# Kernel tuning notes

Measured on AMD Instinct MI355X. Metric: run time of the kernel, lower is better.

The kernel has to match this reference:

```python
import jax, jax.numpy as jnp
import numpy as np

B, T, S, D, H = 2, 2048, 2048, 2048, 16
HD = D // H  # 128
SCALE = 1.0 / np.sqrt(HD)


def _rope(x, cos, sin):
    # x: [B,H,S,HD]; cos/sin: [1,1,S,HD//2]
    b, h, s, d = x.shape
    xs = x.reshape(b, h, s, d // 2, 2)
    x0, x1 = xs[..., 0], xs[..., 1]
    rot = jnp.stack([x0 * cos - x1 * sin, x1 * cos + x0 * sin], axis=-1)
    return rot.reshape(b, h, s, d)


def _split_heads(x):
    b, s, _ = x.shape
    return x.reshape(b, s, H, HD).transpose(0, 2, 1, 3)


def setup_inputs() -> dict:
    key = jax.random.key(0)
    ks = jax.random.split(key, 6)
    w_std = (1.0 / np.sqrt(2.0)) * np.sqrt(6.0 / (D + D))  # xavier_uniform with gain 1/sqrt(2)
    def xavier(k):
        return jax.random.uniform(k, (D, D), jnp.float32, -w_std, w_std)
    # rotary tables (standard inv-freq form)
    inv_freq = 1.0 / (10000.0 ** (np.arange(0, HD, 2, dtype=np.float32) / HD))  # [HD//2]
    ang = np.arange(T, dtype=np.float32)[:, None] * inv_freq[None, :]           # [T,HD//2]
    cos = jnp.asarray(np.cos(ang), jnp.float32)[None, None]  # [1,1,T,HD//2]
    sin = jnp.asarray(np.sin(ang), jnp.float32)[None, None]
    return {
        "hidden_states": jax.random.normal(ks[0], (B, T, D), jnp.float32),
        "encoder_hidden_states": jax.random.normal(ks[1], (B, S, D), jnp.float32),
        "Wq": xavier(ks[2]),
        "Wk": xavier(ks[3]),
        "Wv": xavier(ks[4]),
        "Wo": xavier(ks[5]),
        "cos_q": cos, "sin_q": sin,
        "cos_k": cos, "sin_k": sin,
    }


def reference(hidden_states, encoder_hidden_states, Wq, Wk, Wv, Wo,
              cos_q, sin_q, cos_k, sin_k):
    # Linear (no bias): y = x @ W.T
    q = _split_heads(jnp.einsum('btd,ed->bte', hidden_states, Wq))          # [B,H,T,HD]
    k = _split_heads(jnp.einsum('bsd,ed->bse', encoder_hidden_states, Wk))  # [B,H,S,HD]
    v = _split_heads(jnp.einsum('bsd,ed->bse', encoder_hidden_states, Wv))  # [B,H,S,HD]
    q = _rope(q, cos_q, sin_q)
    k = _rope(k, cos_k, sin_k)
    scores = jnp.einsum('bhtd,bhsd->bhts', q, k) * SCALE                    # [B,H,T,S]
    attn = jax.nn.softmax(scores.astype(jnp.float32), axis=-1)
    ctx = jnp.einsum('bhts,bhsd->bhtd', attn, v)                            # [B,H,T,HD]
    ctx = ctx.transpose(0, 2, 1, 3).reshape(B, T, D)                        # merge heads
    return jnp.einsum('btd,ed->bte', ctx, Wo)
```

## Files before the change

### kernel.cpp

```cpp
#include <hip/hip_runtime.h>
#include <cmath>

#define SCALE_F 0.088388347648318447f

typedef _Float16 f16;
typedef _Float16 f16x8 __attribute__((ext_vector_type(8)));
typedef float f32x4 __attribute__((ext_vector_type(4)));

#define MFMA16(a, b, c) __builtin_amdgcn_mfma_f32_16x16x32_f16(a, b, c, 0, 0, 0)

__device__ __forceinline__ void gl2lds16(const f16* g, f16* l) {
    __builtin_amdgcn_global_load_lds(
        (const __attribute__((address_space(1))) unsigned int*)g,
        (__attribute__((address_space(3))) unsigned int*)l, 16, 0, 0);
}

__global__ __launch_bounds__(256) void cvt_all(
    const float* __restrict__ hs, const float* __restrict__ es,
    const float* __restrict__ Wq, const float* __restrict__ Wk,
    const float* __restrict__ Wv, const float* __restrict__ Wo,
    f16* __restrict__ dst)
{
    const int c = blockIdx.x * 256 + threadIdx.x;
    const float* src; int off;
    if (c < 2097152) { src = (c < 1048576) ? hs : es; off = c & 1048575; }
    else {
        const int cc = c - 2097152;
        const int wsel = cc >> 19; off = cc & 524287;
        src = wsel == 0 ? Wq : wsel == 1 ? Wk : wsel == 2 ? Wv : Wo;
    }
    const float4* p = (const float4*)src + (size_t)off * 2;
    const float4 a = p[0], b2 = p[1];
    f16x8 o = {(f16)a.x, (f16)a.y, (f16)a.z, (f16)a.w,
               (f16)b2.x, (f16)b2.y, (f16)b2.z, (f16)b2.w};
    *(f16x8*)(dst + (size_t)c * 8) = o;
}

template <int OUT_MODE>
__global__ __launch_bounds__(256, 2) void gemm16(
    const f16* __restrict__ A, const f16* __restrict__ W,
    void* __restrict__ Cv, int M, int N, int K,
    const float* __restrict__ Cs, const float* __restrict__ Sn)
{
    __shared__ __align__(16) f16 Al[128 * 64];
    __shared__ __align__(16) f16 Bl[128 * 64];
    const int tid = threadIdx.x;
    const int l = tid & 63, w = tid >> 6;
    const int wr = w >> 1, wc = w & 1;

    const int nwg = gridDim.x, cpx = nwg >> 3;
    const int bid = blockIdx.x;
    const int swz = (bid & 7) * cpx + (bid >> 3);
    const int nbn = N >> 7;
    const int bm = (swz / nbn) * 128, bn = (swz % nbn) * 128;

    f32x4 acc[4][4];
#pragma unroll
    for (int i = 0; i < 4; ++i)
#pragma unroll
        for (int j = 0; j < 4; ++j) acc[i][j] = (f32x4){0.f, 0.f, 0.f, 0.f};

    const int srow = tid >> 3;
    const int sg = tid & 7;

    for (int k0 = 0; k0 < K; k0 += 64) {
        __syncthreads();
#pragma unroll
        for (int i = 0; i < 4; ++i) {
            const int row = i * 32 + srow;
            const int lg = sg ^ (row & 7);
            gl2lds16(A + (size_t)(bm + row) * K + k0 + lg * 8, Al + row * 64 + sg * 8);
            gl2lds16(W + (size_t)(bn + row) * K + k0 + lg * 8, Bl + row * 64 + sg * 8);
        }
        __syncthreads();
#pragma unroll
        for (int kk = 0; kk < 2; ++kk) {
            f16x8 a[4], b[4];
            const int g = kk * 4 + (l >> 4);
#pragma unroll
            for (int m = 0; m < 4; ++m) {
                const int row = wr * 64 + m * 16 + (l & 15);
                a[m] = *(const f16x8*)(Al + row * 64 + (g ^ (row & 7)) * 8);
            }
#pragma unroll
            for (int n = 0; n < 4; ++n) {
                const int row = wc * 64 + n * 16 + (l & 15);
                b[n] = *(const f16x8*)(Bl + row * 64 + (g ^ (row & 7)) * 8);
            }
#pragma unroll
            for (int m = 0; m < 4; ++m)
#pragma unroll
                for (int n = 0; n < 4; ++n)
                    acc[m][n] = MFMA16(a[m], b[n], acc[m][n]);
        }
    }

#pragma unroll
    for (int m = 0; m < 4; ++m)
#pragma unroll
        for (int n = 0; n < 4; ++n)
#pragma unroll
            for (int j = 0; j < 4; ++j) {
                const int r = bm + wr * 64 + m * 16 + ((l >> 4) << 2) + j;
                const int c = bn + wc * 64 + n * 16 + (l & 15);
                if (OUT_MODE == 0) {
                    ((f16*)Cv)[(size_t)r * N + c] = (f16)acc[m][n][j];
                } else if (OUT_MODE == 2) {
                    ((float*)Cv)[(size_t)r * N + c] = acc[m][n][j];
                } else if (OUT_MODE == 3) {
                    ((f16*)Cv)[(size_t)((c >> 11) * 2048 + r) * 2048 + (c & 2047)] = (f16)acc[m][n][j];
                } else if (OUT_MODE == 4) {
                    const float v = acc[m][n][j];
                    const float vp = __shfl_xor(v, 1);
                    const int t = r & 2047;
                    const int i2 = (c & 127) >> 1;
                    const float co = Cs[t * 64 + i2];
                    const float si = Sn[t * 64 + i2];
                    const float y = (c & 1) ? fmaf(v, co, vp * si) : fmaf(v, co, -vp * si);
                    ((f16*)Cv)[(size_t)r * N + c] = (f16)y;
                }
            }
}

__global__ __launch_bounds__(512, 4) void attn16(
    const f16* __restrict__ Qg, const f16* __restrict__ Kg,
    const f16* __restrict__ Vt, f16* __restrict__ Og)
{
    __shared__ __align__(16) f16 Kl[2][64 * 128];
    __shared__ __align__(16) f16 Vl[2][128 * 64];
    __shared__ __align__(16) f16 Pl[8][16 * 64];

    const int tid = threadIdx.x;
    const int l = tid & 63, w = tid >> 6;

    const int bid = blockIdx.x;
    const int swz = (bid & 7) * 64 + (bid >> 3);
    const int bh = swz >> 4, qt = swz & 15;
    const int b = bh >> 4, h = bh & 15;

    const size_t rowQ = (size_t)(b * 2048 + qt * 128 + w * 16 + (l & 15));
    f16x8 qf[4];
#pragma unroll
    for (int kk = 0; kk < 4; ++kk)
        qf[kk] = *(const f16x8*)(Qg + rowQ * 2048 + h * 128 + kk * 32 + (l >> 4) * 8);

    f32x4 o[8];
#pragma unroll
    for (int i = 0; i < 8; ++i) o[i] = (f32x4){0.f, 0.f, 0.f, 0.f};
    float m[4] = {-3.0e38f, -3.0e38f, -3.0e38f, -3.0e38f};
    float s_l[4] = {0.f, 0.f, 0.f, 0.f};

    const f16* Kbase = Kg + (size_t)(b * 2048) * 2048 + h * 128;
    const f16* Vbase = Vt + (size_t)(b * 2048 + h * 128) * 2048;

#define STAGE(buf, st) do {                                                              \
    _Pragma("unroll")                                                                    \
    for (int u = 0; u < 2; ++u) {                                                        \
        const int idx = u * 512 + tid; const int row = idx >> 4, g = idx & 15;           \
        gl2lds16(Kbase + (size_t)((st) + row) * 2048 + (g ^ (row & 15)) * 8,             \
                 &Kl[buf][row * 128 + g * 8]);                                           \
    }                                                                                    \
    _Pragma("unroll")                                                                    \
    for (int u = 0; u < 2; ++u) {                                                        \
        const int idx = u * 512 + tid; const int d = idx >> 3, g = idx & 7;              \
        gl2lds16(Vbase + (size_t)d * 2048 + (st) + (g ^ (d & 7)) * 8,                    \
                 &Vl[buf][d * 64 + g * 8]);                                              \
    }                                                                                    \
} while (0)

    STAGE(0, 0);
    __syncthreads();

    int cur = 0;
    for (int t = 0; t < 32; ++t) {
        if (t < 31) STAGE(cur ^ 1, (t + 1) * 64);
        const f16* Kc = Kl[cur];
        const f16* Vc = Vl[cur];
        f16* Pw = Pl[w];

        f32x4 sc[4];
#pragma unroll
        for (int n = 0; n < 4; ++n) sc[n] = (f32x4){0.f, 0.f, 0.f, 0.f};
#pragma unroll
        for (int kk = 0; kk < 4; ++kk) {
            const int g = kk * 4 + (l >> 4);
#pragma unroll
            for (int n = 0; n < 4; ++n) {
                const int srw = n * 16 + (l & 15);
                const f16x8 kf = *(const f16x8*)(Kc + srw * 128 + (g ^ (srw & 15)) * 8);
                sc[n] = MFMA16(qf[kk], kf, sc[n]);
            }
        }
#pragma unroll
        for (int n = 0; n < 4; ++n) sc[n] *= SCALE_F;

#pragma unroll
        for (int j = 0; j < 4; ++j) {
            float v0 = fmaxf(fmaxf(sc[0][j], sc[1][j]), fmaxf(sc[2][j], sc[3][j]));
            v0 = fmaxf(v0, __shfl_xor(v0, 1));
            v0 = fmaxf(v0, __shfl_xor(v0, 2));
            v0 = fmaxf(v0, __shfl_xor(v0, 4));
            v0 = fmaxf(v0, __shfl_xor(v0, 8));
            if (!__all(v0 <= m[j] + 8.0f)) {
                const float mn = fmaxf(m[j], v0);
                const float cr = __expf(m[j] - mn);
                m[j] = mn;
                s_l[j] *= cr;
#pragma unroll
                for (int nd = 0; nd < 8; ++nd) o[nd][j] *= cr;
            }
            const int q = ((l >> 4) << 2) + j;
            float sum = 0.f;
#pragma unroll
            for (int n = 0; n < 4; ++n) {
                const float p = __expf(sc[n][j] - m[j]);
                sum += p;
                const int s_loc = n * 16 + (l & 15);
                const int phys = (s_loc >> 3) ^ (q & 7);
                Pw[q * 64 + phys * 8 + (s_loc & 7)] = (f16)p;
            }
            sum += __shfl_xor(sum, 1);
            sum += __shfl_xor(sum, 2);
            sum += __shfl_xor(sum, 4);
            sum += __shfl_xor(sum, 8);
            s_l[j] += sum;
        }

#pragma unroll
        for (int kk = 0; kk < 2; ++kk) {
            const int q = l & 15;
            const int g = kk * 4 + (l >> 4);
            const f16x8 pa = *(const f16x8*)(Pw + q * 64 + (g ^ (q & 7)) * 8);
#pragma unroll
            for (int nd = 0; nd < 8; ++nd) {
                const int d = nd * 16 + (l & 15);
                const f16x8 vf = *(const f16x8*)(Vc + d * 64 + (g ^ (d & 7)) * 8);
                o[nd] = MFMA16(pa, vf, o[nd]);
            }
        }
        __syncthreads();
        cur ^= 1;
    }
#undef STAGE

#pragma unroll
    for (int j = 0; j < 4; ++j) {
        const float inv = 1.0f / s_l[j];
        const size_t rowO = (size_t)(b * 2048 + qt * 128 + w * 16 + ((l >> 4) << 2) + j);
#pragma unroll
        for (int nd = 0; nd < 8; ++nd)
            Og[rowO * 2048 + h * 128 + nd * 16 + (l & 15)] = (f16)(o[nd][j] * inv);
    }
}

extern "C" void kernel_launch(void* const* d_in, const int* in_sizes, int n_in,
                              void* d_out, int out_size, void* d_ws, size_t ws_size,
                              hipStream_t stream) {
    const float* hs = (const float*)d_in[0];
    const float* es = (const float*)d_in[1];
    const float* Wq = (const float*)d_in[2];
    const float* Wk = (const float*)d_in[3];
    const float* Wv = (const float*)d_in[4];
    const float* Wo = (const float*)d_in[5];
    const float* cq = (const float*)d_in[6];
    const float* sq = (const float*)d_in[7];
    const float* ck = (const float*)d_in[8];
    const float* sk = (const float*)d_in[9];
    float* out = (float*)d_out;

    f16* hs16 = (f16*)d_ws;
    f16* es16 = hs16 + 8388608;
    f16* Wq16 = es16 + 8388608;
    f16* Wk16 = Wq16 + 4194304;
    f16* Wv16 = Wk16 + 4194304;
    f16* Wo16 = Wv16 + 4194304;
    f16* Q16  = Wo16 + 4194304;
    f16* K16  = Q16 + 8388608;
    f16* Vt16 = K16 + 8388608;
    f16* ctx16 = hs16;

    const dim3 tB(256);
    cvt_all<<<dim3(16384), tB, 0, stream>>>(hs, es, Wq, Wk, Wv, Wo, hs16);

    gemm16<4><<<dim3(512), tB, 0, stream>>>(hs16, Wq16, Q16, 4096, 2048, 2048, cq, sq);
    gemm16<4><<<dim3(512), tB, 0, stream>>>(es16, Wk16, K16, 4096, 2048, 2048, ck, sk);
    gemm16<3><<<dim3(512), tB, 0, stream>>>(Wv16, es16, Vt16, 2048, 4096, 2048, nullptr, nullptr);

    attn16<<<dim3(512), dim3(512), 0, stream>>>(Q16, K16, Vt16, ctx16);

    gemm16<2><<<dim3(512), tB, 0, stream>>>(ctx16, Wo16, out, 4096, 2048, 2048, nullptr, nullptr);
}
```

Before: 325.1 us.

## Rewrite attention with 32x32 MFMA, transposed scores, and register-resident P

The attention kernel switches from 16x16x32 to 32x32x16 MFMA and computes S^T = K·Q^T, so each wave owns 32 query rows and P stays in registers as the A operand of the PV MFMA. This removes the LDS round trip for P. Softmax moves to base-2 with the scale folded into Q, and row reductions use permlane32 swaps instead of shuffle trees. Each block now covers 256 query rows, so the grid is halved to 256 blocks and the occupancy hint drops to one block. Fewer waves hide latency, and setprio hints are added around the MFMA loops.

Result: faster. 303.9 us (-6.5%).

```diff
diff --git a/kernel.cpp b/kernel.cpp
--- a/kernel.cpp
+++ b/kernel.cpp
@@ -5,14 +5,38 @@
 
 typedef _Float16 f16;
 typedef _Float16 f16x8 __attribute__((ext_vector_type(8)));
+typedef _Float16 f16x4 __attribute__((ext_vector_type(4)));
 typedef float f32x4 __attribute__((ext_vector_type(4)));
+typedef float f32x16 __attribute__((ext_vector_type(16)));
+typedef unsigned int u32;
+typedef unsigned int u32x4 __attribute__((ext_vector_type(4)));
 
 #define MFMA16(a, b, c) __builtin_amdgcn_mfma_f32_16x16x32_f16(a, b, c, 0, 0, 0)
+#define MFMA32(a, b, c) __builtin_amdgcn_mfma_f32_32x32x16_f16(a, b, c, 0, 0, 0)
+#define Z16 ((f32x16){0.f,0.f,0.f,0.f,0.f,0.f,0.f,0.f,0.f,0.f,0.f,0.f,0.f,0.f,0.f,0.f})
 
 __device__ __forceinline__ void gl2lds16(const f16* g, f16* l) {
     __builtin_amdgcn_global_load_lds(
         (const __attribute__((address_space(1))) unsigned int*)g,
         (__attribute__((address_space(3))) unsigned int*)l, 16, 0, 0);
+}
+
+__device__ __forceinline__ u32 pk2(float x, float y) {
+    const unsigned short a = __builtin_bit_cast(unsigned short, (f16)x);
+    const unsigned short b = __builtin_bit_cast(unsigned short, (f16)y);
+    return (u32)a | ((u32)b << 16);
+}
+__device__ __forceinline__ float fswapsum(float x) {
+    u32 a = __builtin_bit_cast(u32, x), b;
+    asm volatile("v_mov_b32 %0, %1" : "=&v"(b) : "v"(a));
+    asm volatile("v_permlane32_swap_b32 %0, %1" : "+v"(a), "+v"(b));
+    return __builtin_bit_cast(float, a) + __builtin_bit_cast(float, b);
+}
+__device__ __forceinline__ float fswapmax(float x) {
+    u32 a = __builtin_bit_cast(u32, x), b;
+    asm volatile("v_mov_b32 %0, %1" : "=&v"(b) : "v"(a));
+    asm volatile("v_permlane32_swap_b32 %0, %1" : "+v"(a), "+v"(b));
+    return fmaxf(__builtin_bit_cast(float, a), __builtin_bit_cast(float, b));
 }
 
 __global__ __launch_bounds__(256) void cvt_all(
@@ -122,33 +146,37 @@
             }
 }
 
-__global__ __launch_bounds__(512, 4) void attn16(
+__global__ __launch_bounds__(512, 1) void attn16(
     const f16* __restrict__ Qg, const f16* __restrict__ Kg,
     const f16* __restrict__ Vt, f16* __restrict__ Og)
 {
     __shared__ __align__(16) f16 Kl[2][64 * 128];
     __shared__ __align__(16) f16 Vl[2][128 * 64];
-    __shared__ __align__(16) f16 Pl[8][16 * 64];
+    __shared__ float bnc[8][32];
 
     const int tid = threadIdx.x;
     const int l = tid & 63, w = tid >> 6;
+    const int l31 = l & 31, hi = l >> 5;
+    const int hi4 = hi * 4;
 
     const int bid = blockIdx.x;
-    const int swz = (bid & 7) * 64 + (bid >> 3);
-    const int bh = swz >> 4, qt = swz & 15;
+    const int swz = (bid & 7) * 32 + (bid >> 3);
+    const int bh = swz >> 3, qt = swz & 7;
     const int b = bh >> 4, h = bh & 15;
 
-    const size_t rowQ = (size_t)(b * 2048 + qt * 128 + w * 16 + (l & 15));
-    f16x8 qf[4];
-#pragma unroll
-    for (int kk = 0; kk < 4; ++kk)
-        qf[kk] = *(const f16x8*)(Qg + rowQ * 2048 + h * 128 + kk * 32 + (l >> 4) * 8);
-
-    f32x4 o[8];
-#pragma unroll
-    for (int i = 0; i < 8; ++i) o[i] = (f32x4){0.f, 0.f, 0.f, 0.f};
-    float m[4] = {-3.0e38f, -3.0e38f, -3.0e38f, -3.0e38f};
-    float s_l[4] = {0.f, 0.f, 0.f, 0.f};
+    const int qrow = b * 2048 + qt * 256 + w * 32 + l31;
+    const f16 qsc = (f16)(0.088388347648318447f * 1.44269504088896f);
+    f16x8 qf[8];
+#pragma unroll
+    for (int kc = 0; kc < 8; ++kc) {
+        f16x8 t0 = *(const f16x8*)(Qg + (size_t)qrow * 2048 + h * 128 + kc * 16 + hi * 8);
+#pragma unroll
+        for (int e = 0; e < 8; ++e) t0[e] = t0[e] * qsc;
+        qf[kc] = t0;
+    }
+
+    f32x16 o[4] = {Z16, Z16, Z16, Z16};
+    float mrow = -3.0e38f, lrow = 0.0f;
 
     const f16* Kbase = Kg + (size_t)(b * 2048) * 2048 + h * 128;
     const f16* Vbase = Vt + (size_t)(b * 2048 + h * 128) * 2048;
@@ -176,80 +204,94 @@
         if (t < 31) STAGE(cur ^ 1, (t + 1) * 64);
         const f16* Kc = Kl[cur];
         const f16* Vc = Vl[cur];
-        f16* Pw = Pl[w];
-
-        f32x4 sc[4];
-#pragma unroll
-        for (int n = 0; n < 4; ++n) sc[n] = (f32x4){0.f, 0.f, 0.f, 0.f};
-#pragma unroll
-        for (int kk = 0; kk < 4; ++kk) {
-            const int g = kk * 4 + (l >> 4);
-#pragma unroll
-            for (int n = 0; n < 4; ++n) {
-                const int srw = n * 16 + (l & 15);
-                const f16x8 kf = *(const f16x8*)(Kc + srw * 128 + (g ^ (srw & 15)) * 8);
-                sc[n] = MFMA16(qf[kk], kf, sc[n]);
-            }
-        }
-#pragma unroll
-        for (int n = 0; n < 4; ++n) sc[n] *= SCALE_F;
-
-#pragma unroll
-        for (int j = 0; j < 4; ++j) {
-            float v0 = fmaxf(fmaxf(sc[0][j], sc[1][j]), fmaxf(sc[2][j], sc[3][j]));
-            v0 = fmaxf(v0, __shfl_xor(v0, 1));
-            v0 = fmaxf(v0, __shfl_xor(v0, 2));
-            v0 = fmaxf(v0, __shfl_xor(v0, 4));
-            v0 = fmaxf(v0, __shfl_xor(v0, 8));
-            if (!__all(v0 <= m[j] + 8.0f)) {
-                const float mn = fmaxf(m[j], v0);
-                const float cr = __expf(m[j] - mn);
-                m[j] = mn;
-                s_l[j] *= cr;
-#pragma unroll
-                for (int nd = 0; nd < 8; ++nd) o[nd][j] *= cr;
-            }
-            const int q = ((l >> 4) << 2) + j;
-            float sum = 0.f;
-#pragma unroll
-            for (int n = 0; n < 4; ++n) {
-                const float p = __expf(sc[n][j] - m[j]);
-                sum += p;
-                const int s_loc = n * 16 + (l & 15);
-                const int phys = (s_loc >> 3) ^ (q & 7);
-                Pw[q * 64 + phys * 8 + (s_loc & 7)] = (f16)p;
-            }
-            sum += __shfl_xor(sum, 1);
-            sum += __shfl_xor(sum, 2);
-            sum += __shfl_xor(sum, 4);
-            sum += __shfl_xor(sum, 8);
-            s_l[j] += sum;
-        }
-
-#pragma unroll
-        for (int kk = 0; kk < 2; ++kk) {
-            const int q = l & 15;
-            const int g = kk * 4 + (l >> 4);
-            const f16x8 pa = *(const f16x8*)(Pw + q * 64 + (g ^ (q & 7)) * 8);
-#pragma unroll
-            for (int nd = 0; nd < 8; ++nd) {
-                const int d = nd * 16 + (l & 15);
-                const f16x8 vf = *(const f16x8*)(Vc + d * 64 + (g ^ (d & 7)) * 8);
-                o[nd] = MFMA16(pa, vf, o[nd]);
-            }
-        }
+
+        f32x16 p0 = Z16, p1 = Z16;
+        __builtin_amdgcn_s_setprio(1);
+#pragma unroll
+        for (int kc = 0; kc < 8; ++kc) {
+            const int g = ((kc * 2 + hi) ^ (l31 & 15)) * 8;
+            const f16x8 k0 = *(const f16x8*)(Kc + l31 * 128 + g);
+            const f16x8 k1 = *(const f16x8*)(Kc + (32 + l31) * 128 + g);
+            p0 = MFMA32(k0, qf[kc], p0);
+            p1 = MFMA32(k1, qf[kc], p1);
+        }
+        __builtin_amdgcn_s_setprio(0);
+
+        float mx = fmaxf(p0[0], p1[0]);
+#pragma unroll
+        for (int r = 1; r < 16; ++r) mx = fmaxf(mx, fmaxf(p0[r], p1[r]));
+        mx = fswapmax(mx);
+
+        if (!__all(mx <= mrow + 8.0f)) {
+            const float mn = fmaxf(mrow, mx);
+            const float cr = exp2f(mrow - mn);
+            mrow = mn;
+            lrow *= cr;
+            if (hi == 0) bnc[w][l31] = cr;
+#pragma unroll
+            for (int r = 0; r < 16; ++r) {
+                const float crr = bnc[w][(r & 3) + 8 * (r >> 2) + 4 * hi];
+                o[0][r] *= crr; o[1][r] *= crr; o[2][r] *= crr; o[3][r] *= crr;
+            }
+        }
+
+        float s0 = 0.f, s1 = 0.f, s2 = 0.f, s3 = 0.f;
+#pragma unroll
+        for (int r = 0; r < 16; r += 4) {
+            p0[r]     = exp2f(p0[r]     - mrow); s0 += p0[r];
+            p0[r + 1] = exp2f(p0[r + 1] - mrow); s1 += p0[r + 1];
+            p0[r + 2] = exp2f(p0[r + 2] - mrow); s2 += p0[r + 2];
+            p0[r + 3] = exp2f(p0[r + 3] - mrow); s3 += p0[r + 3];
+        }
+#pragma unroll
+        for (int r = 0; r < 16; r += 4) {
+            p1[r]     = exp2f(p1[r]     - mrow); s0 += p1[r];
+            p1[r + 1] = exp2f(p1[r + 1] - mrow); s1 += p1[r + 1];
+            p1[r + 2] = exp2f(p1[r + 2] - mrow); s2 += p1[r + 2];
+            p1[r + 3] = exp2f(p1[r + 3] - mrow); s3 += p1[r + 3];
+        }
+        lrow += fswapsum((s0 + s1) + (s2 + s3));
+
+        f16x8 pf[4];
+#pragma unroll
+        for (int ksl = 0; ksl < 2; ++ksl) {
+            u32x4 w0 = {pk2(p0[8*ksl+0], p0[8*ksl+1]), pk2(p0[8*ksl+2], p0[8*ksl+3]),
+                        pk2(p0[8*ksl+4], p0[8*ksl+5]), pk2(p0[8*ksl+6], p0[8*ksl+7])};
+            pf[ksl] = __builtin_bit_cast(f16x8, w0);
+            u32x4 w1 = {pk2(p1[8*ksl+0], p1[8*ksl+1]), pk2(p1[8*ksl+2], p1[8*ksl+3]),
+                        pk2(p1[8*ksl+4], p1[8*ksl+5]), pk2(p1[8*ksl+6], p1[8*ksl+7])};
+            pf[2 + ksl] = __builtin_bit_cast(f16x8, w1);
+        }
+
+        __builtin_amdgcn_s_setprio(1);
+#pragma unroll
+        for (int dt = 0; dt < 4; ++dt) {
+            const f16* vrow = Vc + (dt * 32 + l31) * 64;
+#pragma unroll
+            for (int ks = 0; ks < 4; ++ks) {
+                const f16x4 vlo = *(const f16x4*)(vrow + ((ks * 2)     ^ (l31 & 7)) * 8 + hi4);
+                const f16x4 vhi = *(const f16x4*)(vrow + ((ks * 2 + 1) ^ (l31 & 7)) * 8 + hi4);
+                const f16x8 vf = __builtin_shufflevector(vlo, vhi, 0, 1, 2, 3, 4, 5, 6, 7);
+                o[dt] = MFMA32(pf[ks], vf, o[dt]);
+            }
+        }
+        __builtin_amdgcn_s_setprio(0);
+
         __syncthreads();
         cur ^= 1;
     }
 #undef STAGE
 
-#pragma unroll
-    for (int j = 0; j < 4; ++j) {
-        const float inv = 1.0f / s_l[j];
-        const size_t rowO = (size_t)(b * 2048 + qt * 128 + w * 16 + ((l >> 4) << 2) + j);
-#pragma unroll
-        for (int nd = 0; nd < 8; ++nd)
-            Og[rowO * 2048 + h * 128 + nd * 16 + (l & 15)] = (f16)(o[nd][j] * inv);
+    const float inv = 1.0f / lrow;
+    if (hi == 0) bnc[w][l31] = inv;
+#pragma unroll
+    for (int r = 0; r < 16; ++r) {
+        const int qq = (r & 3) + 8 * (r >> 2) + 4 * hi;
+        const float ir = bnc[w][qq];
+        const size_t row = (size_t)(b * 2048 + qt * 256 + w * 32 + qq);
+#pragma unroll
+        for (int dt = 0; dt < 4; ++dt)
+            Og[row * 2048 + h * 128 + dt * 32 + l31] = (f16)(o[dt][r] * ir);
     }
 }
 
@@ -286,7 +328,7 @@
     gemm16<4><<<dim3(512), tB, 0, stream>>>(es16, Wk16, K16, 4096, 2048, 2048, ck, sk);
     gemm16<3><<<dim3(512), tB, 0, stream>>>(Wv16, es16, Vt16, 2048, 4096, 2048, nullptr, nullptr);
 
-    attn16<<<dim3(512), dim3(512), 0, stream>>>(Q16, K16, Vt16, ctx16);
+    attn16<<<dim3(256), dim3(512), 0, stream>>>(Q16, K16, Vt16, ctx16);
 
     gemm16<2><<<dim3(512), tB, 0, stream>>>(ctx16, Wo16, out, 4096, 2048, 2048, nullptr, nullptr);
 }
```
